# Kernel optimization log

Measured on AMD Instinct MI355X. Metric: run time of the kernel, lower is better.

The kernel has to match this reference:

```python
import jax, jax.numpy as jnp
import numpy as np

B, S, H, UNITS = 32, 2048, 1024, 1024


def setup_inputs() -> dict:
    key = jax.random.key(0)
    ks = jax.random.split(key, 5)
    scale = 1.0 / np.sqrt(H)
    return {
        "query": jax.random.normal(ks[0], (B, H), dtype=jnp.float32),
        "values": jax.random.normal(ks[1], (B, S, H), dtype=jnp.float32),
        "W1": jax.random.normal(ks[2], (H, UNITS), dtype=jnp.float32) * scale,
        "b1": jnp.zeros((UNITS,), dtype=jnp.float32),
        "W2": jax.random.normal(ks[3], (H, UNITS), dtype=jnp.float32) * scale,
        "b2": jnp.zeros((UNITS,), dtype=jnp.float32),
        "V": jax.random.normal(ks[4], (UNITS, 1), dtype=jnp.float32) * (1.0 / np.sqrt(UNITS)),
        "bV": jnp.zeros((1,), dtype=jnp.float32),
    }


def reference(query, values, W1, b1, W2, b2, V, bV):
    # W1(values): [B,S,U]; W2(query): [B,1,U] broadcast over S
    proj_v = jnp.einsum("bsh,hu->bsu", values, W1) + b1
    proj_q = (query @ W2 + b2)[:, None, :]
    score = jnp.tanh(proj_v + proj_q) @ V + bV          # [B,S,1]
    attention_weights = jax.nn.softmax(score, axis=1)   # softmax over seq
    context_vector = jnp.sum(attention_weights * values, axis=1)  # [B,H]
    return (attention_weights, context_vector)
```

## Files before the change

kernel.cpp:

```cpp
#include <hip/hip_runtime.h>
#include <hip/hip_bf16.h>
#include <stdint.h>

#define B_ 32
#define S_ 2048
#define H_ 1024
#define U_ 1024

typedef __attribute__((ext_vector_type(8))) short short8;
typedef __attribute__((ext_vector_type(4))) float f32x4;

#define AS1 __attribute__((address_space(1)))
#define AS3 __attribute__((address_space(3)))
#define FENCE __builtin_amdgcn_sched_barrier(0)

__device__ __forceinline__ unsigned short f2bf(float f) {
  unsigned int u = __float_as_uint(f);
  u += 0x7fffu + ((u >> 16) & 1u);
  return (unsigned short)(u >> 16);
}
__device__ __forceinline__ float bf2f(unsigned short s) {
  return __uint_as_float(((unsigned int)s) << 16);
}

__global__ void k_cvt(const float* __restrict__ v, unsigned short* __restrict__ o) {
  const size_t n = (size_t)B_ * S_ * H_;
  const size_t stride = (size_t)gridDim.x * blockDim.x * 8;
  for (size_t i = ((size_t)blockIdx.x * blockDim.x + threadIdx.x) * 8; i < n; i += stride) {
    float4 a = *(const float4*)(v + i), b = *(const float4*)(v + i + 4);
    short8 w;
    w[0]=f2bf(a.x); w[1]=f2bf(a.y); w[2]=f2bf(a.z); w[3]=f2bf(a.w);
    w[4]=f2bf(b.x); w[5]=f2bf(b.y); w[6]=f2bf(b.z); w[7]=f2bf(b.w);
    *(short8*)(o + i) = w;
  }
}

__global__ void k_transpose_w1(const float* __restrict__ W1, unsigned short* __restrict__ W1T) {
  __shared__ float tile[64][65];
  const int tx = threadIdx.x, ty = threadIdx.y;
  const int u0 = blockIdx.x * 64, h0 = blockIdx.y * 64;
#pragma unroll
  for (int i = 0; i < 16; ++i) {
    int hl = ty + i * 4;
    tile[hl][tx] = W1[(size_t)(h0 + hl) * U_ + (u0 + tx)];
  }
  __syncthreads();
#pragma unroll
  for (int i = 0; i < 16; ++i) {
    int ul = ty + i * 4;
    W1T[(size_t)(u0 + ul) * H_ + (h0 + tx)] = f2bf(tile[tx][ul]);
  }
}

__global__ void k_b1q_part(const float* __restrict__ query, const float* __restrict__ W2,
                           float* __restrict__ qpart) {
  __shared__ float q_sh[32 * 128];
  const int u = blockIdx.x * 256 + threadIdx.x;
  const int hs = blockIdx.y;
  for (int i = threadIdx.x; i < 4096; i += 256) {
    const int b = i >> 7, h = i & 127;
    q_sh[i] = query[b * H_ + hs * 128 + h];
  }
  __syncthreads();
  float acc[32];
#pragma unroll
  for (int b = 0; b < 32; ++b) acc[b] = 0.f;
  for (int h = 0; h < 128; ++h) {
    const float w = W2[(size_t)(hs * 128 + h) * U_ + u];
#pragma unroll
    for (int b = 0; b < 32; ++b) acc[b] += q_sh[b * 128 + h] * w;
  }
#pragma unroll
  for (int b = 0; b < 32; ++b) qpart[((size_t)hs * 32 + b) * U_ + u] = acc[b];
}

__global__ void k_b1q_comb(const float* __restrict__ qpart, const float* __restrict__ b1,
                           const float* __restrict__ b2, float* __restrict__ b1q) {
  const int u = blockIdx.x * 256 + threadIdx.x;
  const int b = blockIdx.y;
  float s = b1[u] + b2[u];
#pragma unroll
  for (int hs = 0; hs < 8; ++hs) s += qpart[((size_t)hs * 32 + b) * U_ + u];
  b1q[b * U_ + u] = s;
}

#define BM 128
#define BN 256
#define BK 32
#define NSTEP 32

__global__ __launch_bounds__(512, 4)
void k_fused_score(const unsigned short* __restrict__ vbf,
                   const unsigned short* __restrict__ W1T,
                   const float* __restrict__ b1q, const float* __restrict__ V,
                   float* __restrict__ score_part) {
  __shared__ __align__(16) unsigned char smem[73728];
  unsigned short* As = (unsigned short*)smem;
  unsigned short* Bs = (unsigned short*)(smem + 24576);
  float* scorebuf = (float*)smem;

  const int tid = threadIdx.x;
  const int g = blockIdx.x;
  const int seq = (g & 7) * 256 + (g >> 3);
  const int bn = seq & 3;
  const int bm = seq >> 2;

  const int lane = tid & 63, wid = tid >> 6;
  const int wm = wid >> 2, wn = wid & 3;
  const int u0 = bn * BN;

  const int arow_s = tid >> 2;
  const int alc = (tid & 3) ^ ((arow_s >> 1) & 3);
  const unsigned short* aSrc = vbf + (size_t)(bm * BM + arow_s) * H_ + alc * 8;
  const unsigned short* bSrc0 = W1T + (size_t)(u0 + arow_s) * H_ + alc * 8;
  const unsigned short* bSrc1 = bSrc0 + (size_t)128 * H_;

  const int l15 = lane & 15, l16 = lane >> 4;
  const int fsq = ((l16 ^ ((lane >> 1) & 3)) << 3);
  const int pA = (wm * 64 + l15) * 32 + fsq;
  const int pB = (wn * 64 + l15) * 32 + fsq;

  f32x4 acc[4][4];
#pragma unroll
  for (int mf = 0; mf < 4; ++mf)
#pragma unroll
    for (int nf = 0; nf < 4; ++nf) acc[mf][nf] = (f32x4){0.f, 0.f, 0.f, 0.f};

#define STAGE(tt, slot) { \
    const int ko_ = (tt) * BK; \
    __builtin_amdgcn_global_load_lds((const AS1 void*)(aSrc + ko_), \
        (AS3 void*)&As[(slot) * 4096 + tid * 8], 16, 0, 0); \
    __builtin_amdgcn_global_load_lds((const AS1 void*)(bSrc0 + ko_), \
        (AS3 void*)&Bs[(slot) * 8192 + tid * 8], 16, 0, 0); \
    __builtin_amdgcn_global_load_lds((const AS1 void*)(bSrc1 + ko_), \
        (AS3 void*)&Bs[(slot) * 8192 + 4096 + tid * 8], 16, 0, 0); }

  STAGE(0, 0);
  STAGE(1, 1);
  asm volatile("s_waitcnt vmcnt(3)" ::: "memory");
  FENCE;
  __builtin_amdgcn_s_barrier();

  int slot = 0;
  for (int t = 0; t < NSTEP; ++t) {
    const int nslot = (slot >= 1) ? slot - 1 : 2;
    if (t + 2 < NSTEP) { STAGE(t + 2, nslot); }
    FENCE;
    short8 af[4], bv[4];
#pragma unroll
    for (int mf = 0; mf < 4; ++mf)
      af[mf] = *(const short8*)&As[slot * 4096 + pA + mf * 512];
#pragma unroll
    for (int nf = 0; nf < 4; ++nf)
      bv[nf] = *(const short8*)&Bs[slot * 8192 + pB + nf * 512];
#pragma unroll
    for (int nf = 0; nf < 4; ++nf)
#pragma unroll
      for (int mf = 0; mf < 4; ++mf)
        acc[mf][nf] = __builtin_amdgcn_mfma_f32_16x16x32_bf16(af[mf], bv[nf], acc[mf][nf], 0, 0, 0);
    FENCE;
    if (t + 2 < NSTEP) { asm volatile("s_waitcnt vmcnt(3)" ::: "memory"); }
    else               { asm volatile("s_waitcnt vmcnt(0)" ::: "memory"); }
    FENCE;
    __builtin_amdgcn_s_barrier();
    slot = (slot == 2) ? 0 : slot + 1;
  }

  __syncthreads();
  const int b_blk = bm >> 4;
  float bqv[4], vvv[4];
#pragma unroll
  for (int nf = 0; nf < 4; ++nf) {
    const int ug = u0 + wn * 64 + nf * 16 + l15;
    bqv[nf] = b1q[b_blk * U_ + ug];
    vvv[nf] = V[ug];
  }
  float rp[4][4];
#pragma unroll
  for (int mf = 0; mf < 4; ++mf)
#pragma unroll
    for (int j = 0; j < 4; ++j) rp[mf][j] = 0.f;
#pragma unroll
  for (int nf = 0; nf < 4; ++nf)
#pragma unroll
    for (int mf = 0; mf < 4; ++mf) {
      const f32x4 c = acc[mf][nf];
#pragma unroll
      for (int j = 0; j < 4; ++j) {
        const float x = c[j] + bqv[nf];
        const float e = __expf(2.f * x);
        const float tt = 1.f - 2.f / (e + 1.f);
        rp[mf][j] += tt * vvv[nf];
      }
    }
#pragma unroll
  for (int mf = 0; mf < 4; ++mf)
#pragma unroll
    for (int j = 0; j < 4; ++j) {
      float v = rp[mf][j];
      v += __shfl_xor(v, 1);
      v += __shfl_xor(v, 2);
      v += __shfl_xor(v, 4);
      v += __shfl_xor(v, 8);
      rp[mf][j] = v;
    }
  if (l15 == 0) {
#pragma unroll
    for (int mf = 0; mf < 4; ++mf)
#pragma unroll
      for (int j = 0; j < 4; ++j)
        scorebuf[(wm * 64 + mf * 16 + l16 * 4 + j) * 4 + wn] = rp[mf][j];
  }
  __syncthreads();
  if (tid < BM) {
    const float s = scorebuf[tid * 4 + 0] + scorebuf[tid * 4 + 1] +
                    scorebuf[tid * 4 + 2] + scorebuf[tid * 4 + 3];
    score_part[(size_t)bn * (B_ * S_) + bm * BM + tid] = s;
  }
}

__global__ void k_softmax(const float* __restrict__ sp, float* __restrict__ aw) {
  __shared__ float red[8];
  const int b = blockIdx.x, tid = threadIdx.x;
  const int BS = B_ * S_;
  float x[8];
  float m = -1e30f;
#pragma unroll
  for (int i = 0; i < 8; ++i) {
    const int s = b * S_ + tid + i * 256;
    x[i] = sp[s] + sp[BS + s] + sp[2 * BS + s] + sp[3 * BS + s];
    m = fmaxf(m, x[i]);
  }
#pragma unroll
  for (int off = 32; off; off >>= 1) m = fmaxf(m, __shfl_xor(m, off));
  if ((tid & 63) == 0) red[tid >> 6] = m;
  __syncthreads();
  m = fmaxf(fmaxf(red[0], red[1]), fmaxf(red[2], red[3]));
  float e[8];
  float sum = 0.f;
#pragma unroll
  for (int i = 0; i < 8; ++i) { e[i] = __expf(x[i] - m); sum += e[i]; }
#pragma unroll
  for (int off = 32; off; off >>= 1) sum += __shfl_xor(sum, off);
  __syncthreads();
  if ((tid & 63) == 0) red[4 + (tid >> 6)] = sum;
  __syncthreads();
  sum = red[4] + red[5] + red[6] + red[7];
  const float inv = 1.f / sum;
#pragma unroll
  for (int i = 0; i < 8; ++i) aw[b * S_ + tid + i * 256] = e[i] * inv;
}

__global__ void k_ctx_partial(const unsigned short* __restrict__ vbf, const float* __restrict__ aw,
                              float* __restrict__ part) {
  __shared__ float a_s[128];
  const int b = blockIdx.y, sc = blockIdx.x, tid = threadIdx.x;
  if (tid < 128) a_s[tid] = aw[b * S_ + sc * 128 + tid];
  __syncthreads();
  const unsigned short* vp = vbf + (size_t)(b * S_ + sc * 128) * H_ + tid * 4;
  float4 acc = {0.f, 0.f, 0.f, 0.f};
#pragma unroll 4
  for (int i = 0; i < 128; ++i) {
    const ushort4 v = *(const ushort4*)(vp + (size_t)i * H_);
    const float a = a_s[i];
    acc.x += a * bf2f(v.x); acc.y += a * bf2f(v.y);
    acc.z += a * bf2f(v.z); acc.w += a * bf2f(v.w);
  }
  ((float4*)part)[(size_t)(b * 16 + sc) * (H_ / 4) + tid] = acc;
}

__global__ void k_ctx_combine(const float* __restrict__ part, float* __restrict__ ctx) {
  const int b = blockIdx.x, tid = threadIdx.x;
  float4 s = {0.f, 0.f, 0.f, 0.f};
#pragma unroll
  for (int c = 0; c < 16; ++c) {
    const float4 v = ((const float4*)part)[(size_t)(b * 16 + c) * (H_ / 4) + tid];
    s.x += v.x; s.y += v.y; s.z += v.z; s.w += v.w;
  }
  ((float4*)ctx)[b * (H_ / 4) + tid] = s;
}

extern "C" void kernel_launch(void* const* d_in, const int* in_sizes, int n_in,
                              void* d_out, int out_size, void* d_ws, size_t ws_size,
                              hipStream_t stream) {
  const float* query  = (const float*)d_in[0];
  const float* values = (const float*)d_in[1];
  const float* W1     = (const float*)d_in[2];
  const float* b1     = (const float*)d_in[3];
  const float* W2     = (const float*)d_in[4];
  const float* b2     = (const float*)d_in[5];
  const float* V      = (const float*)d_in[6];

  char* ws = (char*)d_ws;
  unsigned short* W1T = (unsigned short*)ws;
  float* b1q   = (float*)(ws + 2u * 1024u * 1024u);
  float* spart = (float*)(ws + 2u * 1024u * 1024u + 128u * 1024u);
  float* cpart = (float*)(ws + 3u * 1024u * 1024u + 128u * 1024u);
  float* qpart = (float*)(ws + 5u * 1024u * 1024u + 128u * 1024u);
  unsigned short* vbf = (unsigned short*)(ws + 8u * 1024u * 1024u);

  float* aw  = (float*)d_out;
  float* ctx = aw + B_ * S_;

  k_transpose_w1<<<dim3(16, 16), dim3(64, 4), 0, stream>>>(W1, W1T);
  k_b1q_part<<<dim3(4, 8), dim3(256), 0, stream>>>(query, W2, qpart);
  k_b1q_comb<<<dim3(4, 32), dim3(256), 0, stream>>>(qpart, b1, b2, b1q);
  k_cvt<<<dim3(2048), dim3(256), 0, stream>>>(values, vbf);
  k_fused_score<<<dim3(2048), dim3(512), 0, stream>>>(vbf, W1T, b1q, V, spart);
  k_softmax<<<dim3(32), dim3(256), 0, stream>>>(spart, aw);
  k_ctx_partial<<<dim3(16, 32), dim3(256), 0, stream>>>(vbf, aw, cpart);
  k_ctx_combine<<<dim3(32), dim3(256), 0, stream>>>(cpart, ctx);
}
```

Before: 310.0 us.

## Fuse fp32-to-bf16 conversion of values into GEMM A-tile loads, drop cvt pass

Removes the standalone pass that converts values to bf16. The score GEMM now loads fp32 values straight into registers, converts them, and writes them to LDS through a double-buffered A slot, while B keeps the async global-to-LDS triple buffer. The context kernel reads fp32 values directly, with its sequence split doubled to keep the grid large. This removes a full write and reread of a 128MB bf16 copy. In exchange the GEMM reads twice as many A bytes, each repeated across the four N tiles, and adds register-staged conversion work to the main loop.

```diff
diff --git a/kernel.cpp b/kernel.cpp
--- a/kernel.cpp
+++ b/kernel.cpp
@@ -18,21 +18,6 @@
   unsigned int u = __float_as_uint(f);
   u += 0x7fffu + ((u >> 16) & 1u);
   return (unsigned short)(u >> 16);
-}
-__device__ __forceinline__ float bf2f(unsigned short s) {
-  return __uint_as_float(((unsigned int)s) << 16);
-}
-
-__global__ void k_cvt(const float* __restrict__ v, unsigned short* __restrict__ o) {
-  const size_t n = (size_t)B_ * S_ * H_;
-  const size_t stride = (size_t)gridDim.x * blockDim.x * 8;
-  for (size_t i = ((size_t)blockIdx.x * blockDim.x + threadIdx.x) * 8; i < n; i += stride) {
-    float4 a = *(const float4*)(v + i), b = *(const float4*)(v + i + 4);
-    short8 w;
-    w[0]=f2bf(a.x); w[1]=f2bf(a.y); w[2]=f2bf(a.z); w[3]=f2bf(a.w);
-    w[4]=f2bf(b.x); w[5]=f2bf(b.y); w[6]=f2bf(b.z); w[7]=f2bf(b.w);
-    *(short8*)(o + i) = w;
-  }
 }
 
 __global__ void k_transpose_w1(const float* __restrict__ W1, unsigned short* __restrict__ W1T) {
@@ -90,13 +75,13 @@
 #define NSTEP 32
 
 __global__ __launch_bounds__(512, 4)
-void k_fused_score(const unsigned short* __restrict__ vbf,
+void k_fused_score(const float* __restrict__ values,
                    const unsigned short* __restrict__ W1T,
                    const float* __restrict__ b1q, const float* __restrict__ V,
                    float* __restrict__ score_part) {
-  __shared__ __align__(16) unsigned char smem[73728];
+  __shared__ __align__(16) unsigned char smem[65536];
   unsigned short* As = (unsigned short*)smem;
-  unsigned short* Bs = (unsigned short*)(smem + 24576);
+  unsigned short* Bs = (unsigned short*)(smem + 16384);
   float* scorebuf = (float*)smem;
 
   const int tid = threadIdx.x;
@@ -109,10 +94,14 @@
   const int wm = wid >> 2, wn = wid & 3;
   const int u0 = bn * BN;
 
-  const int arow_s = tid >> 2;
-  const int alc = (tid & 3) ^ ((arow_s >> 1) & 3);
-  const unsigned short* aSrc = vbf + (size_t)(bm * BM + arow_s) * H_ + alc * 8;
-  const unsigned short* bSrc0 = W1T + (size_t)(u0 + arow_s) * H_ + alc * 8;
+  const int arow = tid >> 2;
+  const int alc  = tid & 3;
+  const int aplc = alc ^ ((arow >> 1) & 3);
+  const float* aSrcF = values + (size_t)(bm * BM + arow) * H_ + alc * 8;
+  const int awoff = arow * 32 + aplc * 8;
+
+  const int blc = (tid & 3) ^ ((arow >> 1) & 3);
+  const unsigned short* bSrc0 = W1T + (size_t)(u0 + arow) * H_ + blc * 8;
   const unsigned short* bSrc1 = bSrc0 + (size_t)128 * H_;
 
   const int l15 = lane & 15, l16 = lane >> 4;
@@ -126,44 +115,60 @@
 #pragma unroll
     for (int nf = 0; nf < 4; ++nf) acc[mf][nf] = (f32x4){0.f, 0.f, 0.f, 0.f};
 
-#define STAGE(tt, slot) { \
+  float4 ar0, ar1;
+
+#define ISSUE_ARF(tt) { \
+    const float4* p_ = (const float4*)(aSrcF + (tt) * BK); \
+    ar0 = p_[0]; ar1 = p_[1]; }
+
+#define WRITE_ARF(slot) { \
+    short8 w_; \
+    w_[0]=f2bf(ar0.x); w_[1]=f2bf(ar0.y); w_[2]=f2bf(ar0.z); w_[3]=f2bf(ar0.w); \
+    w_[4]=f2bf(ar1.x); w_[5]=f2bf(ar1.y); w_[6]=f2bf(ar1.z); w_[7]=f2bf(ar1.w); \
+    *(short8*)&As[(slot) * 4096 + awoff] = w_; }
+
+#define STAGE_B(tt, slot) { \
     const int ko_ = (tt) * BK; \
-    __builtin_amdgcn_global_load_lds((const AS1 void*)(aSrc + ko_), \
-        (AS3 void*)&As[(slot) * 4096 + tid * 8], 16, 0, 0); \
     __builtin_amdgcn_global_load_lds((const AS1 void*)(bSrc0 + ko_), \
         (AS3 void*)&Bs[(slot) * 8192 + tid * 8], 16, 0, 0); \
     __builtin_amdgcn_global_load_lds((const AS1 void*)(bSrc1 + ko_), \
         (AS3 void*)&Bs[(slot) * 8192 + 4096 + tid * 8], 16, 0, 0); }
 
-  STAGE(0, 0);
-  STAGE(1, 1);
-  asm volatile("s_waitcnt vmcnt(3)" ::: "memory");
+  ISSUE_ARF(0);
+  STAGE_B(0, 0);
+  STAGE_B(1, 1);
+  asm volatile("s_waitcnt vmcnt(4)" ::: "memory");
+  WRITE_ARF(0);
+  asm volatile("s_waitcnt vmcnt(2)" ::: "memory");
+  asm volatile("s_waitcnt lgkmcnt(0)" ::: "memory");
   FENCE;
   __builtin_amdgcn_s_barrier();
 
-  int slot = 0;
   for (int t = 0; t < NSTEP; ++t) {
-    const int nslot = (slot >= 1) ? slot - 1 : 2;
-    if (t + 2 < NSTEP) { STAGE(t + 2, nslot); }
+    const int aslot = t & 1;
+    const int bslot = t % 3;
+    if (t + 1 < NSTEP) { ISSUE_ARF(t + 1); }
+    if (t + 2 < NSTEP) { STAGE_B(t + 2, (t + 2) % 3); }
     FENCE;
     short8 af[4], bv[4];
 #pragma unroll
     for (int mf = 0; mf < 4; ++mf)
-      af[mf] = *(const short8*)&As[slot * 4096 + pA + mf * 512];
+      af[mf] = *(const short8*)&As[aslot * 4096 + pA + mf * 512];
 #pragma unroll
     for (int nf = 0; nf < 4; ++nf)
-      bv[nf] = *(const short8*)&Bs[slot * 8192 + pB + nf * 512];
+      bv[nf] = *(const short8*)&Bs[bslot * 8192 + pB + nf * 512];
 #pragma unroll
     for (int nf = 0; nf < 4; ++nf)
 #pragma unroll
       for (int mf = 0; mf < 4; ++mf)
         acc[mf][nf] = __builtin_amdgcn_mfma_f32_16x16x32_bf16(af[mf], bv[nf], acc[mf][nf], 0, 0, 0);
     FENCE;
-    if (t + 2 < NSTEP) { asm volatile("s_waitcnt vmcnt(3)" ::: "memory"); }
-    else               { asm volatile("s_waitcnt vmcnt(0)" ::: "memory"); }
+    if (t + 2 < NSTEP)      { asm volatile("s_waitcnt vmcnt(2)" ::: "memory"); }
+    else                    { asm volatile("s_waitcnt vmcnt(0)" ::: "memory"); }
+    if (t + 1 < NSTEP) { WRITE_ARF((t + 1) & 1); }
+    asm volatile("s_waitcnt lgkmcnt(0)" ::: "memory");
     FENCE;
     __builtin_amdgcn_s_barrier();
-    slot = (slot == 2) ? 0 : slot + 1;
   }
 
   __syncthreads();
@@ -251,30 +256,29 @@
   for (int i = 0; i < 8; ++i) aw[b * S_ + tid + i * 256] = e[i] * inv;
 }
 
-__global__ void k_ctx_partial(const unsigned short* __restrict__ vbf, const float* __restrict__ aw,
+__global__ void k_ctx_partial(const float* __restrict__ values, const float* __restrict__ aw,
                               float* __restrict__ part) {
-  __shared__ float a_s[128];
+  __shared__ float a_s[64];
   const int b = blockIdx.y, sc = blockIdx.x, tid = threadIdx.x;
-  if (tid < 128) a_s[tid] = aw[b * S_ + sc * 128 + tid];
-  __syncthreads();
-  const unsigned short* vp = vbf + (size_t)(b * S_ + sc * 128) * H_ + tid * 4;
+  if (tid < 64) a_s[tid] = aw[b * S_ + sc * 64 + tid];
+  __syncthreads();
+  const float4* vp = (const float4*)values + (size_t)(b * S_ + sc * 64) * (H_ / 4) + tid;
   float4 acc = {0.f, 0.f, 0.f, 0.f};
 #pragma unroll 4
-  for (int i = 0; i < 128; ++i) {
-    const ushort4 v = *(const ushort4*)(vp + (size_t)i * H_);
+  for (int i = 0; i < 64; ++i) {
+    const float4 v = vp[(size_t)i * (H_ / 4)];
     const float a = a_s[i];
-    acc.x += a * bf2f(v.x); acc.y += a * bf2f(v.y);
-    acc.z += a * bf2f(v.z); acc.w += a * bf2f(v.w);
-  }
-  ((float4*)part)[(size_t)(b * 16 + sc) * (H_ / 4) + tid] = acc;
+    acc.x += a * v.x; acc.y += a * v.y; acc.z += a * v.z; acc.w += a * v.w;
+  }
+  ((float4*)part)[(size_t)(b * 32 + sc) * (H_ / 4) + tid] = acc;
 }
 
 __global__ void k_ctx_combine(const float* __restrict__ part, float* __restrict__ ctx) {
   const int b = blockIdx.x, tid = threadIdx.x;
   float4 s = {0.f, 0.f, 0.f, 0.f};
 #pragma unroll
-  for (int c = 0; c < 16; ++c) {
-    const float4 v = ((const float4*)part)[(size_t)(b * 16 + c) * (H_ / 4) + tid];
+  for (int c = 0; c < 32; ++c) {
+    const float4 v = ((const float4*)part)[(size_t)(b * 32 + c) * (H_ / 4) + tid];
     s.x += v.x; s.y += v.y; s.z += v.z; s.w += v.w;
   }
   ((float4*)ctx)[b * (H_ / 4) + tid] = s;
@@ -295,9 +299,8 @@
   unsigned short* W1T = (unsigned short*)ws;
   float* b1q   = (float*)(ws + 2u * 1024u * 1024u);
   float* spart = (float*)(ws + 2u * 1024u * 1024u + 128u * 1024u);
-  float* cpart = (float*)(ws + 3u * 1024u * 1024u + 128u * 1024u);
-  float* qpart = (float*)(ws + 5u * 1024u * 1024u + 128u * 1024u);
-  unsigned short* vbf = (unsigned short*)(ws + 8u * 1024u * 1024u);
+  float* qpart = (float*)(ws + 3u * 1024u * 1024u + 128u * 1024u);
+  float* cpart = (float*)(ws + 4u * 1024u * 1024u + 256u * 1024u);
 
   float* aw  = (float*)d_out;
   float* ctx = aw + B_ * S_;
@@ -305,9 +308,8 @@
   k_transpose_w1<<<dim3(16, 16), dim3(64, 4), 0, stream>>>(W1, W1T);
   k_b1q_part<<<dim3(4, 8), dim3(256), 0, stream>>>(query, W2, qpart);
   k_b1q_comb<<<dim3(4, 32), dim3(256), 0, stream>>>(qpart, b1, b2, b1q);
-  k_cvt<<<dim3(2048), dim3(256), 0, stream>>>(values, vbf);
-  k_fused_score<<<dim3(2048), dim3(512), 0, stream>>>(vbf, W1T, b1q, V, spart);
+  k_fused_score<<<dim3(2048), dim3(512), 0, stream>>>(values, W1T, b1q, V, spart);
   k_softmax<<<dim3(32), dim3(256), 0, stream>>>(spart, aw);
-  k_ctx_partial<<<dim3(16, 32), dim3(256), 0, stream>>>(vbf, aw, cpart);
+  k_ctx_partial<<<dim3(32, 32), dim3(256), 0, stream>>>(values, aw, cpart);
   k_ctx_combine<<<dim3(32), dim3(256), 0, stream>>>(cpart, ctx);
 }
```

Result: faster. 285.4 us (-7.9%).
